# Performance work log

Hardware: AMD Instinct MI355X
Metric: run time of the kernel (lower is better)

The kernel has to match this reference:

```python
import jax, jax.numpy as jnp
import numpy as np

TOP_K = 2
EPS = 1e-9

def setup_inputs() -> dict:
    key = jax.random.key(0)
    ks = jax.random.split(key, 8)
    B, L, C, F = 64, 512, 3, 300          # batteries, cycles, channels, curve length
    d_model, d_llm, d_ff, E = 512, 4096, 2048, 8
    s = lambda k, sh: jax.random.normal(k, sh, jnp.float32) * 0.02
    return dict(
        cycle_curve_data=jax.random.normal(ks[0], (B, L, C, F), jnp.float32),
        cycle_numbers=jax.random.uniform(ks[1], (B, 1), jnp.float32),
        DKP_embeddings=jax.random.normal(ks[2], (B, d_llm), jnp.float32),
        gate_W1=s(ks[3], (d_llm + 1, d_ff)), gate_b1=jnp.zeros((d_ff,), jnp.float32),
        gate_W2=s(ks[4], (d_ff, E)), gate_b2=jnp.zeros((E,), jnp.float32),
        expert_W=s(ks[5], (E, C * F, d_model)), expert_b=jnp.zeros((E, d_model), jnp.float32),
        gen_W=s(ks[6], (C * F, d_model)), gen_b=jnp.zeros((d_model,), jnp.float32),
    )

def reference(cycle_curve_data, cycle_numbers, DKP_embeddings,
              gate_W1, gate_b1, gate_W2, gate_b2,
              expert_W, expert_b, gen_W, gen_b):
    B, L, C, F = cycle_curve_data.shape
    # router (PatternRouter_two): 2-layer MLP over [DKP embedding ; cycle number]
    g_in = jnp.concatenate([DKP_embeddings, cycle_numbers], axis=-1)   # [B, d_llm+1]
    h = jax.nn.gelu(g_in @ gate_W1 + gate_b1)
    logits = h @ gate_W2 + gate_b2                                     # [B, E]
    # top-k mask on raw logits (as in source), softmax, mask, renormalize
    _, idx = jax.lax.top_k(logits, TOP_K)
    mask = jnp.zeros(logits.shape, bool).at[jnp.arange(B)[:, None], idx].set(True)
    p = jax.nn.softmax(logits, axis=1)
    g = jnp.where(mask, p, 0.0)
    gates = g / (jnp.sum(g, axis=1, keepdims=True) + EPS)              # [B, E]
    # experts: flatten(start_dim=2) then Linear(3*F -> d_model); combine is linear
    # so fold gates into a per-battery weight: sum_e gates[b,e] * W_e
    x = cycle_curve_data.reshape(B, L, C * F)                          # [B, L, 3F]
    Wb = jnp.einsum('be,eid->bid', gates, expert_W)                    # [B, 3F, d]
    bb = gates @ expert_b                                              # [B, d]
    moe_out = jnp.einsum('bli,bid->bld', x, Wb) + bb[:, None, :]       # [B, L, d]
    general = x @ gen_W + gen_b                                        # [B, L, d]
    # source casts the combined MoE output to bf16 before adding
    return general + moe_out.astype(jnp.bfloat16)
```

## Files before the change

### kernel.cpp

```cpp
#include <hip/hip_runtime.h>
#include <hip/hip_bf16.h>
#include <stdint.h>

typedef __attribute__((ext_vector_type(8))) short short8;
typedef __attribute__((ext_vector_type(4))) short short4v;
typedef __attribute__((ext_vector_type(4))) float f32x4;

__device__ inline unsigned short f2bf(float f) {
    union { float f; uint32_t u; } v; v.f = f;
    uint32_t u = v.u;
    uint32_t r = (u + 0x7FFFu + ((u >> 16) & 1u)) >> 16;
    return (unsigned short)r;
}

__device__ inline short8 pk8(float4 a, float4 b) {
    short8 r;
    r[0] = (short)f2bf(a.x); r[1] = (short)f2bf(a.y);
    r[2] = (short)f2bf(a.z); r[3] = (short)f2bf(a.w);
    r[4] = (short)f2bf(b.x); r[5] = (short)f2bf(b.y);
    r[6] = (short)f2bf(b.z); r[7] = (short)f2bf(b.w);
    return r;
}

__global__ __launch_bounds__(256) void router1(const float* __restrict__ DKP,
                                               const float* __restrict__ W1,
                                               float* __restrict__ part) {
    __shared__ float gin[16 * 64];
    const int t  = threadIdx.x;
    const int g  = blockIdx.x;
    const int jc = g & 1;
    const int bg = (g >> 3) & 3;
    const int ks = ((g >> 1) & 3) | ((g >> 5) << 2);
    const int k0 = ks * 64;
    {
        const int bl = t >> 4, q = t & 15;
        *(float4*)(gin + bl * 64 + q * 4) =
            *(const float4*)(DKP + (size_t)(bg * 16 + bl) * 4096 + k0 + q * 4);
    }
    __syncthreads();
    const int ja = jc * 1024 + t * 4;
    f32x4 acc[16];
    #pragma unroll
    for (int bl = 0; bl < 16; ++bl) acc[bl] = (f32x4){0.f, 0.f, 0.f, 0.f};
    f32x4 wcur[8], wnxt[8];
    #pragma unroll
    for (int i = 0; i < 8; ++i)
        wcur[i] = *(const f32x4*)(W1 + (size_t)(k0 + i) * 2048 + ja);
    #pragma unroll 1
    for (int oct = 0; oct < 8; ++oct) {
        const int kk = oct * 8;
        if (oct < 7) {
            #pragma unroll
            for (int i = 0; i < 8; ++i)
                wnxt[i] = *(const f32x4*)(W1 + (size_t)(k0 + kk + 8 + i) * 2048 + ja);
        }
        #pragma unroll
        for (int bl = 0; bl < 16; ++bl) {
            float4 g0 = *(const float4*)(gin + bl * 64 + kk);
            float4 g1 = *(const float4*)(gin + bl * 64 + kk + 4);
            f32x4 a = acc[bl];
            a = a + wcur[0] * g0.x + wcur[1] * g0.y + wcur[2] * g0.z + wcur[3] * g0.w
                  + wcur[4] * g1.x + wcur[5] * g1.y + wcur[6] * g1.z + wcur[7] * g1.w;
            acc[bl] = a;
        }
        #pragma unroll
        for (int i = 0; i < 8; ++i) wcur[i] = wnxt[i];
    }
    #pragma unroll 1
    for (int bl = 0; bl < 16; ++bl)
        *(f32x4*)(part + ((size_t)(ks * 64 + bg * 16 + bl)) * 2048 + ja) = acc[bl];
}

__global__ __launch_bounds__(256) void router2p(const float* __restrict__ part,
                                                const float* __restrict__ cyc,
                                                const float* __restrict__ W1,
                                                const float* __restrict__ b1,
                                                const float* __restrict__ W2,
                                                float* __restrict__ plog) {
    __shared__ float red[256 * 8];
    const int b = blockIdx.x, jc = blockIdx.y;
    const int t = threadIdx.x;
    const int j = jc * 256 + t;
    float s = 0.f;
    #pragma unroll 8
    for (int tt = 0; tt < 64; ++tt)
        s += part[((size_t)tt * 64 + b) * 2048 + j];
    s += cyc[b] * W1[(size_t)4096 * 2048 + j] + b1[j];
    const float u  = s + 0.044715f * s * s * s;
    const float th = tanhf(0.7978845608028654f * u);
    const float hv = 0.5f * s * (1.0f + th);
    const float* w = W2 + (size_t)j * 8;
    #pragma unroll
    for (int e = 0; e < 8; ++e) red[t * 8 + e] = hv * w[e];
    __syncthreads();
    if (t < 8) {
        float acc = 0.f;
        for (int r = 0; r < 256; ++r) acc += red[r * 8 + t];
        plog[((size_t)b * 8 + jc) * 8 + t] = acc;
    }
}

__global__ __launch_bounds__(64) void router4(const float* __restrict__ plog,
                                              const float* __restrict__ b2,
                                              float4* __restrict__ gates) {
    const int b = threadIdx.x;
    float l[8];
    #pragma unroll
    for (int e = 0; e < 8; ++e) l[e] = b2[e];
    #pragma unroll
    for (int jc = 0; jc < 8; ++jc)
        #pragma unroll
        for (int e = 0; e < 8; ++e)
            l[e] += plog[((size_t)b * 8 + jc) * 8 + e];
    int e0 = 0;
    #pragma unroll
    for (int e = 1; e < 8; ++e) if (l[e] > l[e0]) e0 = e;
    int e1 = (e0 == 0) ? 1 : 0;
    #pragma unroll
    for (int e = 0; e < 8; ++e) if (e != e0 && l[e] > l[e1]) e1 = e;
    const float m = l[e0];
    float p[8], Z = 0.f;
    #pragma unroll
    for (int e = 0; e < 8; ++e) { p[e] = expf(l[e] - m); Z += p[e]; }
    const float pe0 = p[e0] / Z, pe1 = p[e1] / Z;
    const float s2 = pe0 + pe1 + 1e-9f;
    gates[b] = make_float4(__int_as_float(e0), __int_as_float(e1), pe0 / s2, pe1 / s2);
}

__global__ __launch_bounds__(256) void combine_w(const float* __restrict__ genW,
                                                 const float* __restrict__ expW,
                                                 const float4* __restrict__ gates,
                                                 unsigned short* __restrict__ wc) {
    __shared__ float T[9][32 * 36];
    __shared__ float4 gsh[64];
    const int t  = threadIdx.x;
    const int d0 = blockIdx.x * 32;
    const int kt = blockIdx.y;
    const int i0 = kt * 32;
    if (t < 64) gsh[t] = gates[t];
    {
        const int il = t >> 3, d4 = (t & 7) * 4;
        const int i = i0 + il;
        const bool valid = (i < 900);
        const size_t off = (size_t)i * 512 + d0 + d4;
        #pragma unroll
        for (int s = 0; s < 9; ++s) {
            const float* src = (s == 0) ? genW : (expW + (size_t)(s - 1) * 900 * 512);
            float4 v = valid ? *(const float4*)(src + off) : make_float4(0, 0, 0, 0);
            float* Td = &T[s][0];
            Td[(d4 + 0) * 36 + il] = v.x;
            Td[(d4 + 1) * 36 + il] = v.y;
            Td[(d4 + 2) * 36 + il] = v.z;
            Td[(d4 + 3) * 36 + il] = v.w;
        }
    }
    __syncthreads();
    const int bb = t >> 7;
    const int dl = (t >> 2) & 31;
    const int sg = t & 3;
    const int fo = dl * 36 + sg * 8;
    unsigned short* wrow = wc + (size_t)kt * 16384 + (d0 + dl) * 32 + sg * 8;
    #pragma unroll 2
    for (int bp = 0; bp < 32; ++bp) {
        const int b = bp * 2 + bb;
        const float4 gt = gsh[b];
        const int e0 = __float_as_int(gt.x), e1 = __float_as_int(gt.y);
        const float g0 = gt.z, g1 = gt.w;
        float4 Ga = *(const float4*)&T[0][fo],      Gb = *(const float4*)&T[0][fo + 4];
        float4 Xa = *(const float4*)&T[1 + e0][fo], Xb = *(const float4*)&T[1 + e0][fo + 4];
        float4 Ya = *(const float4*)&T[1 + e1][fo], Yb = *(const float4*)&T[1 + e1][fo + 4];
        short8 r;
        r[0] = (short)f2bf(Ga.x + g0 * Xa.x + g1 * Ya.x);
        r[1] = (short)f2bf(Ga.y + g0 * Xa.y + g1 * Ya.y);
        r[2] = (short)f2bf(Ga.z + g0 * Xa.z + g1 * Ya.z);
        r[3] = (short)f2bf(Ga.w + g0 * Xa.w + g1 * Ya.w);
        r[4] = (short)f2bf(Gb.x + g0 * Xb.x + g1 * Yb.x);
        r[5] = (short)f2bf(Gb.y + g0 * Xb.y + g1 * Yb.y);
        r[6] = (short)f2bf(Gb.z + g0 * Xb.z + g1 * Yb.z);
        r[7] = (short)f2bf(Gb.w + g0 * Xb.w + g1 * Yb.w);
        *(short8*)(wrow + (size_t)b * 475136) = r;
    }
}

__global__ __launch_bounds__(512, 1) void moe_gemm(const float* __restrict__ x,
                                                   const unsigned short* __restrict__ wc,
                                                   const float4* __restrict__ gates,
                                                   const float* __restrict__ eb,
                                                   const float* __restrict__ genb,
                                                   float* __restrict__ out) {
    __shared__ unsigned short As[2][128 * 40];
    __shared__ unsigned short Bs[2][512 * 32];
    const int g  = blockIdx.x;
    const int b  = (g & 7) + 8 * (g >> 5);
    const int m0 = ((g >> 3) & 3) * 128;
    const int t = threadIdx.x, lane = t & 63, wid = t >> 6;
    const float4 gt = gates[b];
    const int e0 = __float_as_int(gt.x), e1 = __float_as_int(gt.y);
    const float g0 = gt.z, g1 = gt.w;
    const float* xb = x + (size_t)b * 512 * 900;
    const unsigned short* wcb = wc + (size_t)b * 475136;
    f32x4 acc[4][8];
    #pragma unroll
    for (int mi = 0; mi < 4; ++mi)
        #pragma unroll
        for (int ni = 0; ni < 8; ++ni)
            acc[mi][ni] = (f32x4){0.f, 0.f, 0.f, 0.f};

    const int arow = t >> 2;
    const int acol = (t & 3) * 8;
    const float* xrow = xb + (size_t)(m0 + arow) * 900 + acol;
    const int bseg  = (lane & 3) ^ ((lane >> 3) & 3);
    const int burow = lane >> 2;

    const int wm = wid >> 2;
    const int wn = (wid & 3) * 128;
    const int lm = lane & 15, lq = lane >> 4;

    auto stageB = [&](int buf, int kt) {
        const unsigned short* slab = wcb + (size_t)kt * 16384;
        #pragma unroll
        for (int r = 0; r < 4; ++r) {
            const int chunk = wid * 4 + r;
            const unsigned short* gsrc = slab + (chunk * 16 + burow) * 32 + bseg * 8;
            unsigned short* ldst = &Bs[buf][chunk * 512];
            __builtin_amdgcn_global_load_lds(
                (const __attribute__((address_space(1))) unsigned int*)gsrc,
                (__attribute__((address_space(3))) unsigned int*)ldst, 16, 0, 0);
        }
    };
    auto loadA = [&](int kt, float4& lo, float4& hi) {
        if (kt < 28) {
            lo = *(const float4*)(xrow + kt * 32);
            hi = *(const float4*)(xrow + kt * 32 + 4);
        } else {
            lo = make_float4(0.f, 0.f, 0.f, 0.f);
            hi = make_float4(0.f, 0.f, 0.f, 0.f);
            if (acol == 0) lo = *(const float4*)(xb + (size_t)(m0 + arow) * 900 + 896);
        }
    };
    auto packA = [&](int buf, float4 lo, float4 hi) {
        *(short8*)&As[buf][arow * 40 + acol] = pk8(lo, hi);
    };
    auto compute = [&](int buf) {
        short8 af[4];
        #pragma unroll
        for (int mi = 0; mi < 4; ++mi)
            af[mi] = *(const short8*)&As[buf][(wm * 64 + mi * 16 + lm) * 40 + lq * 8];
        #pragma unroll
        for (int ni = 0; ni < 8; ++ni) {
            const int n = wn + ni * 16 + lm;
            const int slot = lq ^ ((lm >> 1) & 3);
            short8 bf = *(const short8*)&Bs[buf][n * 32 + slot * 8];
            #pragma unroll
            for (int mi = 0; mi < 4; ++mi)
                acc[mi][ni] = __builtin_amdgcn_mfma_f32_16x16x32_bf16(
                    af[mi], bf, acc[mi][ni], 0, 0, 0);
        }
    };

    {
        float4 lo, hi;
        loadA(0, lo, hi);
        stageB(0, 0);
        packA(0, lo, hi);
        __syncthreads();
    }
    #pragma unroll 1
    for (int p = 0; p < 14; ++p) {
        {
            float4 lo, hi;
            loadA(2 * p + 1, lo, hi);
            stageB(1, 2 * p + 1);
            compute(0);
            packA(1, lo, hi);
            __syncthreads();
        }
        {
            float4 lo, hi;
            loadA(2 * p + 2, lo, hi);
            stageB(0, 2 * p + 2);
            compute(1);
            packA(0, lo, hi);
            __syncthreads();
        }
    }
    compute(0);

    #pragma unroll
    for (int ni = 0; ni < 8; ++ni) {
        const int col = wn + ni * 16 + lm;
        const float bias = genb[col] + g0 * eb[e0 * 512 + col] + g1 * eb[e1 * 512 + col];
        #pragma unroll
        for (int mi = 0; mi < 4; ++mi) {
            const int row = m0 + wm * 64 + mi * 16 + lq * 4;
            #pragma unroll
            for (int r = 0; r < 4; ++r)
                out[((size_t)b * 512 + row + r) * 512 + col] = acc[mi][ni][r] + bias;
        }
    }
}

extern "C" void kernel_launch(void* const* d_in, const int* in_sizes, int n_in,
                              void* d_out, int out_size, void* d_ws, size_t ws_size,
                              hipStream_t stream) {
    const float* x    = (const float*)d_in[0];
    const float* cyc  = (const float*)d_in[1];
    const float* dkp  = (const float*)d_in[2];
    const float* gW1  = (const float*)d_in[3];
    const float* gb1  = (const float*)d_in[4];
    const float* gW2  = (const float*)d_in[5];
    const float* gb2  = (const float*)d_in[6];
    const float* eW   = (const float*)d_in[7];
    const float* eb   = (const float*)d_in[8];
    const float* genW = (const float*)d_in[9];
    const float* genb = (const float*)d_in[10];
    float* out = (float*)d_out;

    char* ws = (char*)d_ws;
    unsigned short* wcomb = (unsigned short*)ws;
    float* part  = (float*)ws;
    float4* gts  = (float4*)(ws + 60817408);
    float* plog  = (float*)(ws + 60817408 + 1024);

    router1<<<512, 256, 0, stream>>>(dkp, gW1, part);
    router2p<<<dim3(64, 8), 256, 0, stream>>>(part, cyc, gW1, gb1, gW2, plog);
    router4<<<1, 64, 0, stream>>>(plog, gb2, gts);
    combine_w<<<dim3(16, 29), 256, 0, stream>>>(genW, eW, gts, wcomb);
    moe_gemm<<<256, 512, 0, stream>>>(x, wcomb, gts, eb, genb, out);
}
```

Before: 324.0 us.

## Triple-buffer MoE GEMM pipeline with partial waitcnt barriers, fuse gate finalize into combine

The MoE GEMM moves from double to triple LDS buffering. Each barrier now waits with a partial vmcnt so async B loads for upcoming tiles stay in flight, and A packing is deferred one stage. The router's top-k/softmax kernel is folded into combine_w, where every block recomputes the gates redundantly, which saves one launch. The workspace layout is also separated so the router partials no longer alias the combined weights when space allows. The cost is more LDS use per block and tricky hand-written waitcnt correctness.

```diff
diff --git a/kernel.cpp b/kernel.cpp
--- a/kernel.cpp
+++ b/kernel.cpp
@@ -100,36 +100,11 @@
     }
 }
 
-__global__ __launch_bounds__(64) void router4(const float* __restrict__ plog,
-                                              const float* __restrict__ b2,
-                                              float4* __restrict__ gates) {
-    const int b = threadIdx.x;
-    float l[8];
-    #pragma unroll
-    for (int e = 0; e < 8; ++e) l[e] = b2[e];
-    #pragma unroll
-    for (int jc = 0; jc < 8; ++jc)
-        #pragma unroll
-        for (int e = 0; e < 8; ++e)
-            l[e] += plog[((size_t)b * 8 + jc) * 8 + e];
-    int e0 = 0;
-    #pragma unroll
-    for (int e = 1; e < 8; ++e) if (l[e] > l[e0]) e0 = e;
-    int e1 = (e0 == 0) ? 1 : 0;
-    #pragma unroll
-    for (int e = 0; e < 8; ++e) if (e != e0 && l[e] > l[e1]) e1 = e;
-    const float m = l[e0];
-    float p[8], Z = 0.f;
-    #pragma unroll
-    for (int e = 0; e < 8; ++e) { p[e] = expf(l[e] - m); Z += p[e]; }
-    const float pe0 = p[e0] / Z, pe1 = p[e1] / Z;
-    const float s2 = pe0 + pe1 + 1e-9f;
-    gates[b] = make_float4(__int_as_float(e0), __int_as_float(e1), pe0 / s2, pe1 / s2);
-}
-
 __global__ __launch_bounds__(256) void combine_w(const float* __restrict__ genW,
                                                  const float* __restrict__ expW,
-                                                 const float4* __restrict__ gates,
+                                                 const float* __restrict__ plog,
+                                                 const float* __restrict__ b2,
+                                                 float4* __restrict__ gts,
                                                  unsigned short* __restrict__ wc) {
     __shared__ float T[9][32 * 36];
     __shared__ float4 gsh[64];
@@ -137,7 +112,32 @@
     const int d0 = blockIdx.x * 32;
     const int kt = blockIdx.y;
     const int i0 = kt * 32;
-    if (t < 64) gsh[t] = gates[t];
+    if (t < 64) {
+        const int b = t;
+        float l[8];
+        #pragma unroll
+        for (int e = 0; e < 8; ++e) l[e] = b2[e];
+        #pragma unroll
+        for (int jc = 0; jc < 8; ++jc)
+            #pragma unroll
+            for (int e = 0; e < 8; ++e)
+                l[e] += plog[((size_t)b * 8 + jc) * 8 + e];
+        int e0 = 0;
+        #pragma unroll
+        for (int e = 1; e < 8; ++e) if (l[e] > l[e0]) e0 = e;
+        int e1 = (e0 == 0) ? 1 : 0;
+        #pragma unroll
+        for (int e = 0; e < 8; ++e) if (e != e0 && l[e] > l[e1]) e1 = e;
+        const float m = l[e0];
+        float p[8], Z = 0.f;
+        #pragma unroll
+        for (int e = 0; e < 8; ++e) { p[e] = expf(l[e] - m); Z += p[e]; }
+        const float pe0 = p[e0] / Z, pe1 = p[e1] / Z;
+        const float s2 = pe0 + pe1 + 1e-9f;
+        float4 gv = make_float4(__int_as_float(e0), __int_as_float(e1), pe0 / s2, pe1 / s2);
+        gsh[b] = gv;
+        if (blockIdx.x == 0 && blockIdx.y == 0) gts[b] = gv;
+    }
     {
         const int il = t >> 3, d4 = (t & 7) * 4;
         const int i = i0 + il;
@@ -188,8 +188,8 @@
                                                    const float* __restrict__ eb,
                                                    const float* __restrict__ genb,
                                                    float* __restrict__ out) {
-    __shared__ unsigned short As[2][128 * 40];
-    __shared__ unsigned short Bs[2][512 * 32];
+    __shared__ unsigned short As[3][128 * 40];
+    __shared__ unsigned short Bs[3][512 * 32];
     const int g  = blockIdx.x;
     const int b  = (g & 7) + 8 * (g >> 5);
     const int m0 = ((g >> 3) & 3) * 128;
@@ -229,13 +229,14 @@
         }
     };
     auto loadA = [&](int kt, float4& lo, float4& hi) {
-        if (kt < 28) {
-            lo = *(const float4*)(xrow + kt * 32);
-            hi = *(const float4*)(xrow + kt * 32 + 4);
-        } else {
-            lo = make_float4(0.f, 0.f, 0.f, 0.f);
+        const float* base = (kt < 28) ? (xrow + kt * 32)
+                                      : (xb + (size_t)(m0 + arow) * 900 + 896);
+        const int hoff = (kt < 28) ? 4 : 0;
+        lo = *(const float4*)base;
+        hi = *(const float4*)(base + hoff);
+        if (kt >= 28) {
+            if (acol != 0) lo = make_float4(0.f, 0.f, 0.f, 0.f);
             hi = make_float4(0.f, 0.f, 0.f, 0.f);
-            if (acol == 0) lo = *(const float4*)(xb + (size_t)(m0 + arow) * 900 + 896);
         }
     };
     auto packA = [&](int buf, float4 lo, float4 hi) {
@@ -258,33 +259,31 @@
         }
     };
 
-    {
-        float4 lo, hi;
-        loadA(0, lo, hi);
-        stageB(0, 0);
-        packA(0, lo, hi);
-        __syncthreads();
-    }
+#define BARN(n) asm volatile("s_waitcnt vmcnt(" #n ") lgkmcnt(0)\n\ts_barrier" ::: "memory")
+#define FENCE() asm volatile("" ::: "memory")
+
+    float4 aL, aH, nL, nH;
+    loadA(0, aL, aH);
+    stageB(0, 0);
+    packA(0, aL, aH);
+    BARN(0);
+    loadA(1, aL, aH);
+    stageB(1, 1);
+    FENCE();
     #pragma unroll 1
-    for (int p = 0; p < 14; ++p) {
-        {
-            float4 lo, hi;
-            loadA(2 * p + 1, lo, hi);
-            stageB(1, 2 * p + 1);
-            compute(0);
-            packA(1, lo, hi);
-            __syncthreads();
-        }
-        {
-            float4 lo, hi;
-            loadA(2 * p + 2, lo, hi);
-            stageB(0, 2 * p + 2);
-            compute(1);
-            packA(0, lo, hi);
-            __syncthreads();
-        }
+    for (int q = 0; q < 9; ++q) {
+        const int tb = q * 3;
+        { loadA(tb + 2, nL, nH); stageB(2, tb + 2); compute(0); packA(1, aL, aH); aL = nL; aH = nH; BARN(6); }
+        { loadA(tb + 3, nL, nH); stageB(0, tb + 3); compute(1); packA(2, aL, aH); aL = nL; aH = nH; BARN(6); }
+        { loadA(tb + 4, nL, nH); stageB(1, tb + 4); compute(2); packA(0, aL, aH); aL = nL; aH = nH; BARN(6); }
     }
     compute(0);
+    packA(1, aL, aH);
+    BARN(0);
+    compute(1);
+
+#undef BARN
+#undef FENCE
 
     #pragma unroll
     for (int ni = 0; ni < 8; ++ni) {
@@ -317,14 +316,22 @@
     float* out = (float*)d_out;
 
     char* ws = (char*)d_ws;
+    const size_t WCOMB_BYTES = 60817408ull;
+    const size_t PART_BYTES  = 64ull * 64 * 2048 * 4;
     unsigned short* wcomb = (unsigned short*)ws;
-    float* part  = (float*)ws;
-    float4* gts  = (float4*)(ws + 60817408);
-    float* plog  = (float*)(ws + 60817408 + 1024);
+    float* part; float4* gts; float* plog;
+    if (ws_size >= WCOMB_BYTES + PART_BYTES + (1u << 20)) {
+        part = (float*)(ws + WCOMB_BYTES);
+        gts  = (float4*)(ws + WCOMB_BYTES + PART_BYTES);
+        plog = (float*)(ws + WCOMB_BYTES + PART_BYTES + 1024);
+    } else {
+        part = (float*)ws;
+        gts  = (float4*)(ws + WCOMB_BYTES);
+        plog = (float*)(ws + WCOMB_BYTES + 1024);
+    }
 
     router1<<<512, 256, 0, stream>>>(dkp, gW1, part);
     router2p<<<dim3(64, 8), 256, 0, stream>>>(part, cyc, gW1, gb1, gW2, plog);
-    router4<<<1, 64, 0, stream>>>(plog, gb2, gts);
-    combine_w<<<dim3(16, 29), 256, 0, stream>>>(genW, eW, gts, wcomb);
+    combine_w<<<dim3(16, 29), 256, 0, stream>>>(genW, eW, plog, gb2, gts, wcomb);
     moe_gemm<<<256, 512, 0, stream>>>(x, wcomb, gts, eb, genb, out);
 }
```

New measurement: 322.9 us. Within noise of the previous version (-0.4%).

## Fuse gate combine and top-k routing into GEMM; stage per-batch weights on the fly

Applied to the files above, without the earlier changes.

Removes the per-battery combined bf16 weight materialization (64 copies of a 900x512 matrix) and the separate router4 kernel. A new prep_src kernel instead transposes general and expert weights into a shared fp32 tiled layout. Each GEMM block computes its own top-2 gates from the router logits, then builds its B tile in registers as G + g0*E0 + g1*E1 before packing it to bf16 in LDS. This cuts a large global write and read of combined weights, but each block now reads three fp32 sources per tile through registers instead of using async global-to-LDS loads.

```diff
diff --git a/kernel.cpp b/kernel.cpp
--- a/kernel.cpp
+++ b/kernel.cpp
@@ -20,6 +20,47 @@
     r[4] = (short)f2bf(b.x); r[5] = (short)f2bf(b.y);
     r[6] = (short)f2bf(b.z); r[7] = (short)f2bf(b.w);
     return r;
+}
+
+__device__ inline short8 pk8v(f32x4 a, f32x4 b) {
+    short8 r;
+    r[0] = (short)f2bf(a[0]); r[1] = (short)f2bf(a[1]);
+    r[2] = (short)f2bf(a[2]); r[3] = (short)f2bf(a[3]);
+    r[4] = (short)f2bf(b[0]); r[5] = (short)f2bf(b[1]);
+    r[6] = (short)f2bf(b[2]); r[7] = (short)f2bf(b[3]);
+    return r;
+}
+
+__global__ __launch_bounds__(256) void prep_src(const float* __restrict__ genW,
+                                                const float* __restrict__ expW,
+                                                float* __restrict__ srcs) {
+    __shared__ float T[9][32 * 36];
+    const int t  = threadIdx.x;
+    const int d0 = blockIdx.x * 32;
+    const int kt = blockIdx.y;
+    const int i0 = kt * 32;
+    {
+        const int il = t >> 3, d4 = (t & 7) * 4;
+        const int i = i0 + il;
+        const bool valid = (i < 900);
+        const size_t off = (size_t)i * 512 + d0 + d4;
+        #pragma unroll
+        for (int s = 0; s < 9; ++s) {
+            const float* src = (s == 0) ? genW : (expW + (size_t)(s - 1) * 900 * 512);
+            float4 v = valid ? *(const float4*)(src + off) : make_float4(0, 0, 0, 0);
+            float* Td = &T[s][0];
+            Td[(d4 + 0) * 36 + il] = v.x;
+            Td[(d4 + 1) * 36 + il] = v.y;
+            Td[(d4 + 2) * 36 + il] = v.z;
+            Td[(d4 + 3) * 36 + il] = v.w;
+        }
+    }
+    __syncthreads();
+    const int dl = t >> 3, sg = t & 7;
+    float* base = srcs + (size_t)kt * 16384 + (size_t)(d0 + dl) * 32 + sg * 4;
+    #pragma unroll
+    for (int s = 0; s < 9; ++s)
+        *(float4*)(base + (size_t)s * 475136) = *(const float4*)&T[s][dl * 36 + sg * 4];
 }
 
 __global__ __launch_bounds__(256) void router1(const float* __restrict__ DKP,
@@ -100,105 +141,59 @@
     }
 }
 
-__global__ __launch_bounds__(64) void router4(const float* __restrict__ plog,
-                                              const float* __restrict__ b2,
-                                              float4* __restrict__ gates) {
-    const int b = threadIdx.x;
-    float l[8];
-    #pragma unroll
-    for (int e = 0; e < 8; ++e) l[e] = b2[e];
-    #pragma unroll
-    for (int jc = 0; jc < 8; ++jc)
-        #pragma unroll
-        for (int e = 0; e < 8; ++e)
-            l[e] += plog[((size_t)b * 8 + jc) * 8 + e];
-    int e0 = 0;
-    #pragma unroll
-    for (int e = 1; e < 8; ++e) if (l[e] > l[e0]) e0 = e;
-    int e1 = (e0 == 0) ? 1 : 0;
-    #pragma unroll
-    for (int e = 0; e < 8; ++e) if (e != e0 && l[e] > l[e1]) e1 = e;
-    const float m = l[e0];
-    float p[8], Z = 0.f;
-    #pragma unroll
-    for (int e = 0; e < 8; ++e) { p[e] = expf(l[e] - m); Z += p[e]; }
-    const float pe0 = p[e0] / Z, pe1 = p[e1] / Z;
-    const float s2 = pe0 + pe1 + 1e-9f;
-    gates[b] = make_float4(__int_as_float(e0), __int_as_float(e1), pe0 / s2, pe1 / s2);
-}
-
-__global__ __launch_bounds__(256) void combine_w(const float* __restrict__ genW,
-                                                 const float* __restrict__ expW,
-                                                 const float4* __restrict__ gates,
-                                                 unsigned short* __restrict__ wc) {
-    __shared__ float T[9][32 * 36];
-    __shared__ float4 gsh[64];
-    const int t  = threadIdx.x;
-    const int d0 = blockIdx.x * 32;
-    const int kt = blockIdx.y;
-    const int i0 = kt * 32;
-    if (t < 64) gsh[t] = gates[t];
-    {
-        const int il = t >> 3, d4 = (t & 7) * 4;
-        const int i = i0 + il;
-        const bool valid = (i < 900);
-        const size_t off = (size_t)i * 512 + d0 + d4;
-        #pragma unroll
-        for (int s = 0; s < 9; ++s) {
-            const float* src = (s == 0) ? genW : (expW + (size_t)(s - 1) * 900 * 512);
-            float4 v = valid ? *(const float4*)(src + off) : make_float4(0, 0, 0, 0);
-            float* Td = &T[s][0];
-            Td[(d4 + 0) * 36 + il] = v.x;
-            Td[(d4 + 1) * 36 + il] = v.y;
-            Td[(d4 + 2) * 36 + il] = v.z;
-            Td[(d4 + 3) * 36 + il] = v.w;
-        }
-    }
-    __syncthreads();
-    const int bb = t >> 7;
-    const int dl = (t >> 2) & 31;
-    const int sg = t & 3;
-    const int fo = dl * 36 + sg * 8;
-    unsigned short* wrow = wc + (size_t)kt * 16384 + (d0 + dl) * 32 + sg * 8;
-    #pragma unroll 2
-    for (int bp = 0; bp < 32; ++bp) {
-        const int b = bp * 2 + bb;
-        const float4 gt = gsh[b];
-        const int e0 = __float_as_int(gt.x), e1 = __float_as_int(gt.y);
-        const float g0 = gt.z, g1 = gt.w;
-        float4 Ga = *(const float4*)&T[0][fo],      Gb = *(const float4*)&T[0][fo + 4];
-        float4 Xa = *(const float4*)&T[1 + e0][fo], Xb = *(const float4*)&T[1 + e0][fo + 4];
-        float4 Ya = *(const float4*)&T[1 + e1][fo], Yb = *(const float4*)&T[1 + e1][fo + 4];
-        short8 r;
-        r[0] = (short)f2bf(Ga.x + g0 * Xa.x + g1 * Ya.x);
-        r[1] = (short)f2bf(Ga.y + g0 * Xa.y + g1 * Ya.y);
-        r[2] = (short)f2bf(Ga.z + g0 * Xa.z + g1 * Ya.z);
-        r[3] = (short)f2bf(Ga.w + g0 * Xa.w + g1 * Ya.w);
-        r[4] = (short)f2bf(Gb.x + g0 * Xb.x + g1 * Yb.x);
-        r[5] = (short)f2bf(Gb.y + g0 * Xb.y + g1 * Yb.y);
-        r[6] = (short)f2bf(Gb.z + g0 * Xb.z + g1 * Yb.z);
-        r[7] = (short)f2bf(Gb.w + g0 * Xb.w + g1 * Yb.w);
-        *(short8*)(wrow + (size_t)b * 475136) = r;
-    }
-}
-
 __global__ __launch_bounds__(512, 1) void moe_gemm(const float* __restrict__ x,
-                                                   const unsigned short* __restrict__ wc,
-                                                   const float4* __restrict__ gates,
+                                                   const float* __restrict__ srcs,
+                                                   const float* __restrict__ plog,
+                                                   const float* __restrict__ b2,
                                                    const float* __restrict__ eb,
                                                    const float* __restrict__ genb,
                                                    float* __restrict__ out) {
     __shared__ unsigned short As[2][128 * 40];
     __shared__ unsigned short Bs[2][512 * 32];
+    __shared__ float lgsh[8];
+    __shared__ float4 gate_sh;
     const int g  = blockIdx.x;
     const int b  = (g & 7) + 8 * (g >> 5);
     const int m0 = ((g >> 3) & 3) * 128;
     const int t = threadIdx.x, lane = t & 63, wid = t >> 6;
-    const float4 gt = gates[b];
+
+    if (wid == 0) {
+        const int e = lane & 7, jc = lane >> 3;
+        float v = plog[(size_t)b * 64 + jc * 8 + e];
+        v += __shfl_xor(v, 8);
+        v += __shfl_xor(v, 16);
+        v += __shfl_xor(v, 32);
+        if (lane < 8) lgsh[e] = v + b2[e];
+    }
+    __syncthreads();
+    if (t == 0) {
+        float l[8];
+        #pragma unroll
+        for (int e = 0; e < 8; ++e) l[e] = lgsh[e];
+        int e0 = 0;
+        #pragma unroll
+        for (int e = 1; e < 8; ++e) if (l[e] > l[e0]) e0 = e;
+        int e1 = (e0 == 0) ? 1 : 0;
+        #pragma unroll
+        for (int e = 0; e < 8; ++e) if (e != e0 && l[e] > l[e1]) e1 = e;
+        const float m = l[e0];
+        float p[8], Z = 0.f;
+        #pragma unroll
+        for (int e = 0; e < 8; ++e) { p[e] = expf(l[e] - m); Z += p[e]; }
+        const float pe0 = p[e0] / Z, pe1 = p[e1] / Z;
+        const float s2 = pe0 + pe1 + 1e-9f;
+        gate_sh = make_float4(__int_as_float(e0), __int_as_float(e1), pe0 / s2, pe1 / s2);
+    }
+    __syncthreads();
+    const float4 gt = gate_sh;
     const int e0 = __float_as_int(gt.x), e1 = __float_as_int(gt.y);
     const float g0 = gt.z, g1 = gt.w;
-    const float* xb = x + (size_t)b * 512 * 900;
-    const unsigned short* wcb = wc + (size_t)b * 475136;
+
+    const float* xb  = x + (size_t)b * 512 * 900;
+    const float* sG  = srcs;
+    const float* sE0 = srcs + (size_t)(1 + e0) * 475136;
+    const float* sE1 = srcs + (size_t)(1 + e1) * 475136;
+
     f32x4 acc[4][8];
     #pragma unroll
     for (int mi = 0; mi < 4; ++mi)
@@ -209,25 +204,16 @@
     const int arow = t >> 2;
     const int acol = (t & 3) * 8;
     const float* xrow = xb + (size_t)(m0 + arow) * 900 + acol;
-    const int bseg  = (lane & 3) ^ ((lane >> 3) & 3);
-    const int burow = lane >> 2;
+    const int bseg = (lane & 3) ^ ((lane >> 3) & 3);
+    size_t foffs[4];
+    #pragma unroll
+    for (int r = 0; r < 4; ++r)
+        foffs[r] = (size_t)((wid * 4 + r) * 16 + (lane >> 2)) * 32 + bseg * 8;
 
     const int wm = wid >> 2;
     const int wn = (wid & 3) * 128;
     const int lm = lane & 15, lq = lane >> 4;
 
-    auto stageB = [&](int buf, int kt) {
-        const unsigned short* slab = wcb + (size_t)kt * 16384;
-        #pragma unroll
-        for (int r = 0; r < 4; ++r) {
-            const int chunk = wid * 4 + r;
-            const unsigned short* gsrc = slab + (chunk * 16 + burow) * 32 + bseg * 8;
-            unsigned short* ldst = &Bs[buf][chunk * 512];
-            __builtin_amdgcn_global_load_lds(
-                (const __attribute__((address_space(1))) unsigned int*)gsrc,
-                (__attribute__((address_space(3))) unsigned int*)ldst, 16, 0, 0);
-        }
-    };
     auto loadA = [&](int kt, float4& lo, float4& hi) {
         if (kt < 28) {
             lo = *(const float4*)(xrow + kt * 32);
@@ -241,6 +227,17 @@
     auto packA = [&](int buf, float4 lo, float4 hi) {
         *(short8*)&As[buf][arow * 40 + acol] = pk8(lo, hi);
     };
+    auto commitB = [&](int buf, int r, const f32x4 G[2], const f32x4 EA[2], const f32x4 EB[2]) {
+        f32x4 lo = G[0] + g0 * EA[0] + g1 * EB[0];
+        f32x4 hi = G[1] + g0 * EA[1] + g1 * EB[1];
+        *(short8*)&Bs[buf][(wid * 4 + r) * 512 + lane * 8] = pk8v(lo, hi);
+    };
+    auto loadSrc = [&](int kt, int r, f32x4 G[2], f32x4 EA[2], f32x4 EB[2]) {
+        const size_t fo = foffs[r] + (size_t)kt * 16384;
+        G[0]  = *(const f32x4*)(sG + fo);   G[1]  = *(const f32x4*)(sG + fo + 4);
+        EA[0] = *(const f32x4*)(sE0 + fo);  EA[1] = *(const f32x4*)(sE0 + fo + 4);
+        EB[0] = *(const f32x4*)(sE1 + fo);  EB[1] = *(const f32x4*)(sE1 + fo + 4);
+    };
     auto compute = [&](int buf) {
         short8 af[4];
         #pragma unroll
@@ -257,32 +254,39 @@
                     af[mi], bf, acc[mi][ni], 0, 0, 0);
         }
     };
+    auto step = [&](int bufC, int bufN, int kt_next) {
+        float4 aLo, aHi;
+        loadA(kt_next, aLo, aHi);
+        f32x4 G0[2], EA0[2], EB0[2], G1v[2], EA1[2], EB1[2];
+        loadSrc(kt_next, 0, G0, EA0, EB0);
+        loadSrc(kt_next, 1, G1v, EA1, EB1);
+        compute(bufC);
+        commitB(bufN, 0, G0, EA0, EB0);
+        commitB(bufN, 1, G1v, EA1, EB1);
+        loadSrc(kt_next, 2, G0, EA0, EB0);
+        loadSrc(kt_next, 3, G1v, EA1, EB1);
+        commitB(bufN, 2, G0, EA0, EB0);
+        commitB(bufN, 3, G1v, EA1, EB1);
+        packA(bufN, aLo, aHi);
+        __syncthreads();
+    };
 
     {
-        float4 lo, hi;
-        loadA(0, lo, hi);
-        stageB(0, 0);
-        packA(0, lo, hi);
+        float4 aLo, aHi;
+        loadA(0, aLo, aHi);
+        f32x4 G[2], EA[2], EB[2];
+        #pragma unroll
+        for (int r = 0; r < 4; ++r) {
+            loadSrc(0, r, G, EA, EB);
+            commitB(0, r, G, EA, EB);
+        }
+        packA(0, aLo, aHi);
         __syncthreads();
     }
     #pragma unroll 1
     for (int p = 0; p < 14; ++p) {
-        {
-            float4 lo, hi;
-            loadA(2 * p + 1, lo, hi);
-            stageB(1, 2 * p + 1);
-            compute(0);
-            packA(1, lo, hi);
-            __syncthreads();
-        }
-        {
-            float4 lo, hi;
-            loadA(2 * p + 2, lo, hi);
-            stageB(0, 2 * p + 2);
-            compute(1);
-            packA(0, lo, hi);
-            __syncthreads();
-        }
+        step(0, 1, 2 * p + 1);
+        step(1, 0, 2 * p + 2);
     }
     compute(0);
 
@@ -317,14 +321,14 @@
     float* out = (float*)d_out;
 
     char* ws = (char*)d_ws;
-    unsigned short* wcomb = (unsigned short*)ws;
-    float* part  = (float*)ws;
-    float4* gts  = (float4*)(ws + 60817408);
-    float* plog  = (float*)(ws + 60817408 + 1024);
-
+    const size_t SRC_BYTES  = 9ull * 29 * 512 * 32 * 4;
+    const size_t PART_BYTES = 64ull * 64 * 2048 * 4;
+    float* srcs = (float*)ws;
+    float* part = (float*)(ws + SRC_BYTES);
+    float* plog = (float*)(ws + SRC_BYTES + PART_BYTES);
+
+    prep_src<<<dim3(16, 29), 256, 0, stream>>>(genW, eW, srcs);
     router1<<<512, 256, 0, stream>>>(dkp, gW1, part);
     router2p<<<dim3(64, 8), 256, 0, stream>>>(part, cyc, gW1, gb1, gW2, plog);
-    router4<<<1, 64, 0, stream>>>(plog, gb2, gts);
-    combine_w<<<dim3(16, 29), 256, 0, stream>>>(genW, eW, gts, wcomb);
-    moe_gemm<<<256, 512, 0, stream>>>(x, wcomb, gts, eb, genb, out);
-}
+    moe_gemm<<<256, 512, 0, stream>>>(x, srcs, plog, gb2, eb, genb, out);
+}
```

New measurement: 358.4 us. 1.11x slower.
